# Performance work log

Hardware: AMD Instinct MI355X
Metric: run time of the kernel (lower is better)

Reference implementation:

```python
import jax, jax.numpy as jnp
import numpy as np

NB = 50000      # nb_classes (rel table is also sized by nb_classes in the source)
ES = 50         # embedding_size
D = ES + 1      # 51
B = 8192        # batch per normal-form loss
MARGIN = 0.0
REG_NORM = 1.0
INF = 5.0


def setup_inputs() -> dict:
    key = jax.random.key(0)
    ks = jax.random.split(key, 11)
    ri = lambda k, shape: jax.random.randint(k, shape, 0, NB)
    return {
        "nf1": ri(ks[0], (B, 3)),
        "nf2": ri(ks[1], (B, 3)),
        "nf3": ri(ks[2], (B, 3)),
        "nf4": ri(ks[3], (B, 3)),
        "top": ri(ks[4], (B,)),
        "nf3_neg": ri(ks[5], (B, 3)),
        "nf_inclusion": ri(ks[6], (B, 2)),
        "nf_chain": ri(ks[7], (B, 3)),
        "radius": ri(ks[8], (B,)),
        "cls_emb": jax.random.normal(ks[9], (NB, D), jnp.float32),
        "rel_emb": jax.random.normal(ks[10], (NB, D * D), jnp.float32) * 0.1,
    }


def _norm(x):
    return jnp.sqrt(jnp.sum(x * x, axis=1))


def _reg(x):
    return jnp.abs(_norm(x) - REG_NORM)


def _bmv(rm, v):  # [B,D,D] @ [B,D] -> [B,D]
    return jnp.einsum('bij,bj->bi', rm, v)


def _nf1_loss(cls_emb, rel_emb, idx):
    c = cls_emb[idx[:, 0]]
    d = cls_emb[idx[:, 2]]
    rm = rel_emb[idx[:, 1]].reshape(-1, D, D)
    cr = _bmv(rm, c)
    dr = _bmv(rm, d)
    rc = jax.nn.relu(cr[:, -1])
    rd = jax.nn.relu(dr[:, -1])
    euc = _norm(dr[:, :-1] - cr[:, :-1])
    dst = jax.nn.relu(euc + rc - rd + MARGIN)
    return dst + _reg(c[:, :-1]) + _reg(d[:, :-1])


def _nf2_loss(cls_emb, idx):
    c = cls_emb[idx[:, 0]]
    d = cls_emb[idx[:, 1]]
    e = cls_emb[idx[:, 2]]
    rc = jax.nn.relu(c[:, -1])
    rd = jax.nn.relu(d[:, -1])
    re = jax.nn.relu(e[:, -1])
    sr = rc + rd
    x1, x2, x3 = c[:, :-1], d[:, :-1], e[:, :-1]
    dst = _norm(x2 - x1)
    dst2 = _norm(x3 - x1)
    dst3 = _norm(x3 - x2)
    rdst = jax.nn.relu(jnp.minimum(rc, rd) - re - MARGIN)
    dst_loss = (jax.nn.relu(dst - sr - MARGIN)
                + jax.nn.relu(dst2 - rc - MARGIN)
                + jax.nn.relu(dst3 - rd - MARGIN)
                + rdst)
    return dst_loss + _reg(x1) + _reg(x2) + _reg(x3)


def _nf3_loss(cls_emb, rel_emb, idx):
    c = cls_emb[idx[:, 0]]
    d = cls_emb[idx[:, 2]]
    rm = rel_emb[idx[:, 1]].reshape(-1, D, D)
    cr = _bmv(rm, c)
    dr = _bmv(rm, d)
    rc = jax.nn.relu(c[:, -1])
    rd = jax.nn.relu(d[:, -1])
    euc = _norm(dr[:, :-1] - cr[:, :-1])
    dst = jax.nn.relu(euc + rc - rd - MARGIN)
    return dst + _reg(c[:, :-1]) + _reg(d[:, :-1])


def _nf4_loss(cls_emb, rel_emb, idx):
    c = cls_emb[idx[:, 1]]
    d = cls_emb[idx[:, 2]]
    rm = rel_emb[idx[:, 0]].reshape(-1, D, D)
    cr = _bmv(rm, c)
    dr = _bmv(rm, d)
    rc = jax.nn.relu(c[:, -1])
    rd = jax.nn.relu(d[:, -1])
    sr = rc + rd
    dst = _norm(dr[:, :-1] - cr[:, :-1])
    dst_loss = jax.nn.relu(dst - sr - MARGIN)
    return dst_loss + _reg(c[:, :-1]) + _reg(d[:, :-1])


def _top_loss(cls_emb, idx):
    d = cls_emb[idx]
    rd = jax.nn.relu(d[:, -1])
    return jnp.abs(rd - INF)


def _nf3_neg_loss(cls_emb, rel_emb, idx):
    c = cls_emb[idx[:, 0]]
    d = cls_emb[idx[:, 2]]
    rm = rel_emb[idx[:, 1]].reshape(-1, D, D)
    cr = _bmv(rm, c)
    dr = _bmv(rm, d)
    rc = jax.nn.relu(c[:, -1])
    rd = jax.nn.relu(d[:, -1])
    euc = _norm(dr[:, :-1] - cr[:, :-1])
    dst = -(euc - rc - rd) + MARGIN
    return dst + _reg(c[:, :-1]) + _reg(d[:, :-1])


def _chain_loss(rel_emb, idx):
    c = rel_emb[idx[:, 0]].reshape(-1, D, D)
    d = rel_emb[idx[:, 1]].reshape(-1, D, D)
    e = rel_emb[idx[:, 2]].reshape(-1, D, D)
    cd = jnp.einsum('bik,bkj->bij', c, d)
    return jnp.mean(jnp.abs(e - cd), axis=(1, 2))


def _radius_loss(cls_emb, idx):
    rd = cls_emb[idx][:, -1]
    return jnp.minimum(jnp.zeros_like(rd), rd)


def reference(nf1, nf2, nf3, nf4, top, nf3_neg, nf_inclusion, nf_chain, radius,
              cls_emb, rel_emb):
    loss1 = _nf1_loss(cls_emb, rel_emb, nf1)
    loss2 = _nf2_loss(cls_emb, nf2)
    loss3 = _nf3_loss(cls_emb, rel_emb, nf3)
    loss4 = _nf4_loss(cls_emb, rel_emb, nf4)
    loss_top = _top_loss(cls_emb, top)
    loss_neg = _nf3_neg_loss(cls_emb, rel_emb, nf3_neg)
    loss6 = _chain_loss(rel_emb, nf_chain)
    loss7 = _radius_loss(cls_emb, radius)
    loss = loss1 + loss2 + loss3 + loss4 + loss_top + loss_neg + loss6 - loss7
    return jnp.mean(loss)
```

## Files before the change

### kernel.cpp

```cpp
#include <hip/hip_runtime.h>
#include <hip/hip_bf16.h>

#define DD 51
#define DM 50
#define BB 8192
#define MM (DD*DD)
#define NBUCKET 1024

__device__ __forceinline__ float wave_sum(float v) {
    #pragma unroll
    for (int off = 32; off; off >>= 1) v += __shfl_xor(v, off);
    return v;
}

__global__ __launch_bounds__(256) void zero_kernel(float* __restrict__ buckets) {
    buckets[blockIdx.x * 256 + threadIdx.x] = 0.f;
}

__global__ __launch_bounds__(128, 8) void matvec_loss_kernel(
    const int* __restrict__ nf1, const int* __restrict__ nf3,
    const int* __restrict__ nf4, const int* __restrict__ nfneg,
    const float* __restrict__ cls,
    const float* __restrict__ rel,
    float* __restrict__ buckets)
{
    int task = blockIdx.x;
    int type = task >> 13;
    int b    = task & (BB - 1);
    int ci, ri, di;
    if (type == 0)      { ci = nf1[3*b];   ri = nf1[3*b+1];   di = nf1[3*b+2]; }
    else if (type == 1) { ci = nf3[3*b];   ri = nf3[3*b+1];   di = nf3[3*b+2]; }
    else if (type == 2) { ri = nf4[3*b];   ci = nf4[3*b+1];   di = nf4[3*b+2]; }
    else                { ci = nfneg[3*b]; ri = nfneg[3*b+1]; di = nfneg[3*b+2]; }

    __shared__ float M[MM];
    __shared__ float sc[DD], sd[DD], scr[DD], sdr[DD];
    int tid  = threadIdx.x;
    int wave = tid >> 6;
    int lane = tid & 63;

    const float* Mg = rel + (size_t)ri * MM;
    #pragma unroll 4
    for (int p = tid; p < MM; p += 128) M[p] = Mg[p];

    if (wave == 0) { if (lane < DD) sc[lane] = cls[(size_t)ci * DD + lane]; }
    else           { if (lane < DD) sd[lane] = cls[(size_t)di * DD + lane]; }
    __syncthreads();

    const float* vec = wave ? sd : sc;
    float acc = 0.f;
    if (lane < DD) {
        const float* row = &M[lane * DD];
        #pragma unroll
        for (int j = 0; j < DD; ++j) acc = fmaf(row[j], vec[j], acc);
        if (wave == 0) scr[lane] = acc; else sdr[lane] = acc;
    }
    __syncthreads();

    if (wave == 0) {
        float cv  = (lane < DM) ? sc[lane]  : 0.f;
        float dv  = (lane < DM) ? sd[lane]  : 0.f;
        float crv = (lane < DM) ? scr[lane] : 0.f;
        float drv = (lane < DM) ? sdr[lane] : 0.f;
        float t  = drv - crv;
        float e2 = wave_sum(t * t);
        float c2 = wave_sum(cv * cv);
        float d2 = wave_sum(dv * dv);
        if (lane == 0) {
            float euc = sqrtf(e2);
            float reg = fabsf(sqrtf(c2) - 1.f) + fabsf(sqrtf(d2) - 1.f);
            float L;
            if (type == 0) {
                float rc = fmaxf(scr[DM], 0.f), rd = fmaxf(sdr[DM], 0.f);
                L = fmaxf(euc + rc - rd, 0.f) + reg;
            } else if (type == 1) {
                float rc = fmaxf(sc[DM], 0.f), rd = fmaxf(sd[DM], 0.f);
                L = fmaxf(euc + rc - rd, 0.f) + reg;
            } else if (type == 2) {
                float rc = fmaxf(sc[DM], 0.f), rd = fmaxf(sd[DM], 0.f);
                L = fmaxf(euc - (rc + rd), 0.f) + reg;
            } else {
                float rc = fmaxf(sc[DM], 0.f), rd = fmaxf(sd[DM], 0.f);
                L = -(euc - rc - rd) + reg;
            }
            atomicAdd(&buckets[task & (NBUCKET - 1)], L);
        }
    }
}

__global__ __launch_bounds__(256, 4) void chain_kernel(
    const int* __restrict__ nfc,
    const float* __restrict__ rel,
    float* __restrict__ buckets)
{
    int b  = blockIdx.x;
    int ic = nfc[3*b], id = nfc[3*b+1], ie = nfc[3*b+2];
    alignas(16) __shared__ float CsT[DD][52];
    alignas(16) __shared__ float Ds [DD][52];
    const float* Cg = rel + (size_t)ic * MM;
    const float* Dg = rel + (size_t)id * MM;
    const float* Eg = rel + (size_t)ie * MM;

    int t = threadIdx.x;
    for (int p = t; p < MM; p += 256) {
        int i = p / DD, j = p - i * DD;
        CsT[j][i] = Cg[p];
        Ds [i][j] = Dg[p];
    }
    __syncthreads();

    float local = 0.f;
    if (t < 169) {
        int ti = t / 13, tj = t - ti * 13;
        int i0 = ti * 4, j0 = tj * 4;
        float acc[4][4];
        #pragma unroll
        for (int r = 0; r < 4; ++r)
            #pragma unroll
            for (int c = 0; c < 4; ++c) acc[r][c] = 0.f;

        #pragma unroll 3
        for (int k = 0; k < DD; ++k) {
            float4 ca = *(const float4*)&CsT[k][i0];
            float4 db = *(const float4*)&Ds [k][j0];
            float a[4]  = {ca.x, ca.y, ca.z, ca.w};
            float bv[4] = {db.x, db.y, db.z, db.w};
            #pragma unroll
            for (int r = 0; r < 4; ++r)
                #pragma unroll
                for (int c = 0; c < 4; ++c)
                    acc[r][c] = fmaf(a[r], bv[c], acc[r][c]);
        }
        #pragma unroll
        for (int r = 0; r < 4; ++r) {
            int i = i0 + r;
            if (i < DD) {
                #pragma unroll
                for (int c = 0; c < 4; ++c) {
                    int j = j0 + c;
                    if (j < DD)
                        local += fabsf(Eg[i * DD + j] - acc[r][c]);
                }
            }
        }
    }
    local = wave_sum(local);
    __shared__ float wsum[4];
    if ((t & 63) == 0) wsum[t >> 6] = local;
    __syncthreads();
    if (t == 0) {
        float s = (wsum[0] + wsum[1] + wsum[2] + wsum[3]) * (1.f / (float)MM);
        atomicAdd(&buckets[b & (NBUCKET - 1)], s);
    }
}

__global__ __launch_bounds__(64) void misc_kernel(
    const int* __restrict__ nf2, const int* __restrict__ top,
    const int* __restrict__ radius,
    const float* __restrict__ cls,
    float* __restrict__ buckets)
{
    int b = blockIdx.x;
    int i0 = nf2[3*b], i1 = nf2[3*b+1], i2 = nf2[3*b+2];
    int lane = threadIdx.x;
    float cv = 0.f, dv = 0.f, ev = 0.f;
    if (lane < DD) {
        cv = cls[(size_t)i0 * DD + lane];
        dv = cls[(size_t)i1 * DD + lane];
        ev = cls[(size_t)i2 * DD + lane];
    }
    float m = (lane < DM) ? 1.f : 0.f;
    float s_dc = wave_sum((dv - cv) * (dv - cv) * m);
    float s_ec = wave_sum((ev - cv) * (ev - cv) * m);
    float s_ed = wave_sum((ev - dv) * (ev - dv) * m);
    float s_c  = wave_sum(cv * cv * m);
    float s_d  = wave_sum(dv * dv * m);
    float s_e  = wave_sum(ev * ev * m);

    float c50 = __shfl(cv, DM), d50 = __shfl(dv, DM), e50 = __shfl(ev, DM);
    if (lane == 0) {
        float rc = fmaxf(c50, 0.f), rd = fmaxf(d50, 0.f), re = fmaxf(e50, 0.f);
        float L = fmaxf(sqrtf(s_dc) - (rc + rd), 0.f)
                + fmaxf(sqrtf(s_ec) - rc, 0.f)
                + fmaxf(sqrtf(s_ed) - rd, 0.f)
                + fmaxf(fminf(rc, rd) - re, 0.f)
                + fabsf(sqrtf(s_c) - 1.f)
                + fabsf(sqrtf(s_d) - 1.f)
                + fabsf(sqrtf(s_e) - 1.f);
        float t50 = cls[(size_t)top[b] * DD + DM];
        L += fabsf(fmaxf(t50, 0.f) - 5.f);
        float r50 = cls[(size_t)radius[b] * DD + DM];
        L -= fminf(r50, 0.f);
        atomicAdd(&buckets[b & (NBUCKET - 1)], L);
    }
}

__global__ __launch_bounds__(256) void finalize_kernel(
    const float* __restrict__ buckets, float* __restrict__ out)
{
    int t = threadIdx.x;
    float v = buckets[t] + buckets[t + 256] + buckets[t + 512] + buckets[t + 768];
    v = wave_sum(v);
    __shared__ float ws[4];
    if ((t & 63) == 0) ws[t >> 6] = v;
    __syncthreads();
    if (t == 0) out[0] = (ws[0] + ws[1] + ws[2] + ws[3]) * (1.f / (float)BB);
}

extern "C" void kernel_launch(void* const* d_in, const int* in_sizes, int n_in,
                              void* d_out, int out_size, void* d_ws, size_t ws_size,
                              hipStream_t stream) {
    const int* nf1     = (const int*)d_in[0];
    const int* nf2     = (const int*)d_in[1];
    const int* nf3     = (const int*)d_in[2];
    const int* nf4     = (const int*)d_in[3];
    const int* top     = (const int*)d_in[4];
    const int* nf3n    = (const int*)d_in[5];
    const int* nfc     = (const int*)d_in[7];
    const int* radius  = (const int*)d_in[8];
    const float* cls   = (const float*)d_in[9];
    const float* rel   = (const float*)d_in[10];

    float* buckets = (float*)d_ws;

    zero_kernel<<<NBUCKET / 256, 256, 0, stream>>>(buckets);
    matvec_loss_kernel<<<4 * BB, 128, 0, stream>>>(nf1, nf3, nf4, nf3n, cls, rel, buckets);
    chain_kernel<<<BB, 256, 0, stream>>>(nfc, rel, buckets);
    misc_kernel<<<BB, 64, 0, stream>>>(nf2, top, radius, cls, buckets);
    finalize_kernel<<<1, 256, 0, stream>>>(buckets, (float*)d_out);
}
```

Measured before the change: 740.1 us.

## Use linearity to do one matvec per task and shrink blocks to one wave

The matvec loss kernel now computes M·(d−c) as a single matvec, since only the difference of the two products is needed. The relation-based radius terms come from dot products with row 50. The misc normal-form work is folded into the same launch as a fifth task type. Each block is now one 64-lane wave using padded LDS rows, float4 reads and a multiply-based divide-by-51. The chain kernel also moves to one wave computing 8x8 tiles, staging the product in LDS and then reading E coalesced. The aims are fewer FMAs, fewer barriers and launches, and coalesced E reads, at the cost of more per-thread register pressure and serialised staging loads.

Result: faster. 715.6 us (-3.3%).

```diff
diff --git a/kernel.cpp b/kernel.cpp
--- a/kernel.cpp
+++ b/kernel.cpp
@@ -1,8 +1,8 @@
 #include <hip/hip_runtime.h>
-#include <hip/hip_bf16.h>
 
 #define DD 51
 #define DM 50
+#define PD 52
 #define BB 8192
 #define MM (DD*DD)
 #define NBUCKET 1024
@@ -13,186 +13,210 @@
     return v;
 }
 
+__device__ __forceinline__ int div51(int p) {
+    return (int)((((unsigned long long)(unsigned)p) * 84215046ull) >> 32);
+}
+
 __global__ __launch_bounds__(256) void zero_kernel(float* __restrict__ buckets) {
     buckets[blockIdx.x * 256 + threadIdx.x] = 0.f;
 }
 
-__global__ __launch_bounds__(128, 8) void matvec_loss_kernel(
+__global__ __launch_bounds__(64, 2) void taskA_kernel(
     const int* __restrict__ nf1, const int* __restrict__ nf3,
     const int* __restrict__ nf4, const int* __restrict__ nfneg,
+    const int* __restrict__ nf2, const int* __restrict__ top,
+    const int* __restrict__ radius,
     const float* __restrict__ cls,
     const float* __restrict__ rel,
     float* __restrict__ buckets)
 {
-    int task = blockIdx.x;
-    int type = task >> 13;
-    int b    = task & (BB - 1);
-    int ci, ri, di;
-    if (type == 0)      { ci = nf1[3*b];   ri = nf1[3*b+1];   di = nf1[3*b+2]; }
-    else if (type == 1) { ci = nf3[3*b];   ri = nf3[3*b+1];   di = nf3[3*b+2]; }
-    else if (type == 2) { ri = nf4[3*b];   ci = nf4[3*b+1];   di = nf4[3*b+2]; }
-    else                { ci = nfneg[3*b]; ri = nfneg[3*b+1]; di = nfneg[3*b+2]; }
-
-    __shared__ float M[MM];
-    __shared__ float sc[DD], sd[DD], scr[DD], sdr[DD];
-    int tid  = threadIdx.x;
-    int wave = tid >> 6;
-    int lane = tid & 63;
-
-    const float* Mg = rel + (size_t)ri * MM;
-    #pragma unroll 4
-    for (int p = tid; p < MM; p += 128) M[p] = Mg[p];
-
-    if (wave == 0) { if (lane < DD) sc[lane] = cls[(size_t)ci * DD + lane]; }
-    else           { if (lane < DD) sd[lane] = cls[(size_t)di * DD + lane]; }
-    __syncthreads();
-
-    const float* vec = wave ? sd : sc;
-    float acc = 0.f;
-    if (lane < DD) {
-        const float* row = &M[lane * DD];
+    alignas(16) __shared__ float Mw[DD * PD];
+    alignas(16) __shared__ float vb[PD];
+    const int task = blockIdx.x;
+    const int type = task >> 13;
+    const int b    = task & (BB - 1);
+    const int lane = threadIdx.x;
+
+    if (type < 4) {
+        int ci, ri, di;
+        if (type == 0)      { ci = nf1[3*b];   ri = nf1[3*b+1];   di = nf1[3*b+2]; }
+        else if (type == 1) { ci = nf3[3*b];   ri = nf3[3*b+1];   di = nf3[3*b+2]; }
+        else if (type == 2) { ri = nf4[3*b];   ci = nf4[3*b+1];   di = nf4[3*b+2]; }
+        else                { ci = nfneg[3*b]; ri = nfneg[3*b+1]; di = nfneg[3*b+2]; }
+
+        float cv = 0.f, dv = 0.f;
+        if (lane < DD) {
+            cv = cls[(size_t)ci * DD + lane];
+            dv = cls[(size_t)di * DD + lane];
+        }
+        if (lane < PD) vb[lane] = (lane < DD) ? (dv - cv) : 0.f;
+        if (lane < DD) Mw[lane * PD + (PD - 1)] = 0.f;
+
+        const float* Mg = rel + (size_t)ri * MM;
         #pragma unroll
-        for (int j = 0; j < DD; ++j) acc = fmaf(row[j], vec[j], acc);
-        if (wave == 0) scr[lane] = acc; else sdr[lane] = acc;
-    }
-    __syncthreads();
-
-    if (wave == 0) {
-        float cv  = (lane < DM) ? sc[lane]  : 0.f;
-        float dv  = (lane < DM) ? sd[lane]  : 0.f;
-        float crv = (lane < DM) ? scr[lane] : 0.f;
-        float drv = (lane < DM) ? sdr[lane] : 0.f;
-        float t  = drv - crv;
-        float e2 = wave_sum(t * t);
-        float c2 = wave_sum(cv * cv);
-        float d2 = wave_sum(dv * dv);
+        for (int k = 0; k < 40; ++k) {
+            int p = lane + (k << 6);
+            Mw[p + div51(p)] = Mg[p];
+        }
+        { int p = lane + 2560; if (p < MM) Mw[p + div51(p)] = Mg[p]; }
+        __syncthreads();
+
+        float acc = 0.f;
+        if (lane < DD) {
+            const float4* rp = (const float4*)(Mw + lane * PD);
+            const float4* vp = (const float4*)vb;
+            #pragma unroll
+            for (int q = 0; q < 13; ++q) {
+                float4 a = rp[q], w = vp[q];
+                acc = fmaf(a.x, w.x, acc);
+                acc = fmaf(a.y, w.y, acc);
+                acc = fmaf(a.z, w.z, acc);
+                acc = fmaf(a.w, w.w, acc);
+            }
+        }
+        float mk = (lane < DM) ? 1.f : 0.f;
+        float e2 = wave_sum(acc * acc * mk);
+        float c2 = wave_sum(cv * cv * mk);
+        float d2 = wave_sum(dv * dv * mk);
+        float c50 = __shfl(cv, DM);
+        float d50 = __shfl(dv, DM);
+        float s1 = 0.f, s2 = 0.f;
+        if (type == 0) {
+            float m50 = (lane < DD) ? Mw[DM * PD + lane] : 0.f;
+            s1 = wave_sum(m50 * cv);
+            s2 = wave_sum(m50 * dv);
+        }
         if (lane == 0) {
             float euc = sqrtf(e2);
             float reg = fabsf(sqrtf(c2) - 1.f) + fabsf(sqrtf(d2) - 1.f);
             float L;
             if (type == 0) {
-                float rc = fmaxf(scr[DM], 0.f), rd = fmaxf(sdr[DM], 0.f);
+                float rc = fmaxf(s1, 0.f), rd = fmaxf(s2, 0.f);
                 L = fmaxf(euc + rc - rd, 0.f) + reg;
             } else if (type == 1) {
-                float rc = fmaxf(sc[DM], 0.f), rd = fmaxf(sd[DM], 0.f);
+                float rc = fmaxf(c50, 0.f), rd = fmaxf(d50, 0.f);
                 L = fmaxf(euc + rc - rd, 0.f) + reg;
             } else if (type == 2) {
-                float rc = fmaxf(sc[DM], 0.f), rd = fmaxf(sd[DM], 0.f);
+                float rc = fmaxf(c50, 0.f), rd = fmaxf(d50, 0.f);
                 L = fmaxf(euc - (rc + rd), 0.f) + reg;
             } else {
-                float rc = fmaxf(sc[DM], 0.f), rd = fmaxf(sd[DM], 0.f);
+                float rc = fmaxf(c50, 0.f), rd = fmaxf(d50, 0.f);
                 L = -(euc - rc - rd) + reg;
             }
             atomicAdd(&buckets[task & (NBUCKET - 1)], L);
         }
-    }
-}
-
-__global__ __launch_bounds__(256, 4) void chain_kernel(
+    } else {
+        int i0 = nf2[3*b], i1 = nf2[3*b+1], i2 = nf2[3*b+2];
+        float cv = 0.f, dv = 0.f, ev = 0.f;
+        if (lane < DD) {
+            cv = cls[(size_t)i0 * DD + lane];
+            dv = cls[(size_t)i1 * DD + lane];
+            ev = cls[(size_t)i2 * DD + lane];
+        }
+        float t50 = cls[(size_t)top[b]    * DD + DM];
+        float r50 = cls[(size_t)radius[b] * DD + DM];
+        float m = (lane < DM) ? 1.f : 0.f;
+        float s_dc = wave_sum((dv - cv) * (dv - cv) * m);
+        float s_ec = wave_sum((ev - cv) * (ev - cv) * m);
+        float s_ed = wave_sum((ev - dv) * (ev - dv) * m);
+        float s_c  = wave_sum(cv * cv * m);
+        float s_d  = wave_sum(dv * dv * m);
+        float s_e  = wave_sum(ev * ev * m);
+        float c50 = __shfl(cv, DM), d50 = __shfl(dv, DM), e50 = __shfl(ev, DM);
+        if (lane == 0) {
+            float rc = fmaxf(c50, 0.f), rd = fmaxf(d50, 0.f), re = fmaxf(e50, 0.f);
+            float L = fmaxf(sqrtf(s_dc) - (rc + rd), 0.f)
+                    + fmaxf(sqrtf(s_ec) - rc, 0.f)
+                    + fmaxf(sqrtf(s_ed) - rd, 0.f)
+                    + fmaxf(fminf(rc, rd) - re, 0.f)
+                    + fabsf(sqrtf(s_c) - 1.f)
+                    + fabsf(sqrtf(s_d) - 1.f)
+                    + fabsf(sqrtf(s_e) - 1.f)
+                    + fabsf(fmaxf(t50, 0.f) - 5.f)
+                    - fminf(r50, 0.f);
+            atomicAdd(&buckets[task & (NBUCKET - 1)], L);
+        }
+    }
+}
+
+__global__ __launch_bounds__(64, 2) void chainB_kernel(
     const int* __restrict__ nfc,
     const float* __restrict__ rel,
     float* __restrict__ buckets)
 {
-    int b  = blockIdx.x;
+    alignas(16) __shared__ float lds[2 * DD * PD + 8];
+    float* CsT = lds;
+    float* Dsm = lds + DD * PD;
+    const int b    = blockIdx.x;
+    const int lane = threadIdx.x;
     int ic = nfc[3*b], id = nfc[3*b+1], ie = nfc[3*b+2];
-    alignas(16) __shared__ float CsT[DD][52];
-    alignas(16) __shared__ float Ds [DD][52];
     const float* Cg = rel + (size_t)ic * MM;
     const float* Dg = rel + (size_t)id * MM;
     const float* Eg = rel + (size_t)ie * MM;
 
-    int t = threadIdx.x;
-    for (int p = t; p < MM; p += 256) {
-        int i = p / DD, j = p - i * DD;
-        CsT[j][i] = Cg[p];
-        Ds [i][j] = Dg[p];
-    }
-    __syncthreads();
-
-    float local = 0.f;
-    if (t < 169) {
-        int ti = t / 13, tj = t - ti * 13;
-        int i0 = ti * 4, j0 = tj * 4;
-        float acc[4][4];
+    #pragma unroll 10
+    for (int t = 0; t < 40; ++t) {
+        int p = lane + (t << 6);
+        int r = div51(p), c = p - r * DD;
+        CsT[c * PD + r] = Cg[p];
+        Dsm[p + r]      = Dg[p];
+    }
+    { int p = lane + 2560;
+      if (p < MM) { int r = div51(p), c = p - r * DD; CsT[c*PD + r] = Cg[p]; Dsm[p + r] = Dg[p]; } }
+    __syncthreads();
+
+    int ti = 0, tj = 0;
+    if (lane < 49) { ti = lane / 7; tj = lane - ti * 7; }
+    const int i0 = ti * 8, j0 = tj * 8;
+    float a2[8][8];
+    #pragma unroll
+    for (int r = 0; r < 8; ++r)
         #pragma unroll
-        for (int r = 0; r < 4; ++r)
-            #pragma unroll
-            for (int c = 0; c < 4; ++c) acc[r][c] = 0.f;
-
+        for (int c = 0; c < 8; ++c) a2[r][c] = 0.f;
+
+    if (lane < 49) {
         #pragma unroll 3
         for (int k = 0; k < DD; ++k) {
-            float4 ca = *(const float4*)&CsT[k][i0];
-            float4 db = *(const float4*)&Ds [k][j0];
-            float a[4]  = {ca.x, ca.y, ca.z, ca.w};
-            float bv[4] = {db.x, db.y, db.z, db.w};
+            const float4* cp = (const float4*)(CsT + k * PD + i0);
+            const float4* dp = (const float4*)(Dsm + k * PD + j0);
+            float4 ca0 = cp[0], ca1 = cp[1];
+            float4 db0 = dp[0], db1 = dp[1];
+            float A_[8] = {ca0.x, ca0.y, ca0.z, ca0.w, ca1.x, ca1.y, ca1.z, ca1.w};
+            float B_[8] = {db0.x, db0.y, db0.z, db0.w, db1.x, db1.y, db1.z, db1.w};
             #pragma unroll
-            for (int r = 0; r < 4; ++r)
+            for (int r = 0; r < 8; ++r)
                 #pragma unroll
-                for (int c = 0; c < 4; ++c)
-                    acc[r][c] = fmaf(a[r], bv[c], acc[r][c]);
-        }
+                for (int c = 0; c < 8; ++c)
+                    a2[r][c] = fmaf(A_[r], B_[c], a2[r][c]);
+        }
+    }
+    __syncthreads();
+
+    if (lane < 49) {
         #pragma unroll
-        for (int r = 0; r < 4; ++r) {
+        for (int r = 0; r < 8; ++r) {
             int i = i0 + r;
             if (i < DD) {
-                #pragma unroll
-                for (int c = 0; c < 4; ++c) {
-                    int j = j0 + c;
-                    if (j < DD)
-                        local += fabsf(Eg[i * DD + j] - acc[r][c]);
-                }
+                *(float4*)(lds + i * PD + j0) =
+                    make_float4(a2[r][0], a2[r][1], a2[r][2], a2[r][3]);
+                if (tj < 6)
+                    *(float4*)(lds + i * PD + j0 + 4) =
+                        make_float4(a2[r][4], a2[r][5], a2[r][6], a2[r][7]);
             }
         }
     }
+    __syncthreads();
+
+    float local = 0.f;
+    #pragma unroll 10
+    for (int t = 0; t < 40; ++t) {
+        int p = lane + (t << 6);
+        local += fabsf(Eg[p] - lds[p + div51(p)]);
+    }
+    { int p = lane + 2560; if (p < MM) local += fabsf(Eg[p] - lds[p + div51(p)]); }
     local = wave_sum(local);
-    __shared__ float wsum[4];
-    if ((t & 63) == 0) wsum[t >> 6] = local;
-    __syncthreads();
-    if (t == 0) {
-        float s = (wsum[0] + wsum[1] + wsum[2] + wsum[3]) * (1.f / (float)MM);
-        atomicAdd(&buckets[b & (NBUCKET - 1)], s);
-    }
-}
-
-__global__ __launch_bounds__(64) void misc_kernel(
-    const int* __restrict__ nf2, const int* __restrict__ top,
-    const int* __restrict__ radius,
-    const float* __restrict__ cls,
-    float* __restrict__ buckets)
-{
-    int b = blockIdx.x;
-    int i0 = nf2[3*b], i1 = nf2[3*b+1], i2 = nf2[3*b+2];
-    int lane = threadIdx.x;
-    float cv = 0.f, dv = 0.f, ev = 0.f;
-    if (lane < DD) {
-        cv = cls[(size_t)i0 * DD + lane];
-        dv = cls[(size_t)i1 * DD + lane];
-        ev = cls[(size_t)i2 * DD + lane];
-    }
-    float m = (lane < DM) ? 1.f : 0.f;
-    float s_dc = wave_sum((dv - cv) * (dv - cv) * m);
-    float s_ec = wave_sum((ev - cv) * (ev - cv) * m);
-    float s_ed = wave_sum((ev - dv) * (ev - dv) * m);
-    float s_c  = wave_sum(cv * cv * m);
-    float s_d  = wave_sum(dv * dv * m);
-    float s_e  = wave_sum(ev * ev * m);
-
-    float c50 = __shfl(cv, DM), d50 = __shfl(dv, DM), e50 = __shfl(ev, DM);
-    if (lane == 0) {
-        float rc = fmaxf(c50, 0.f), rd = fmaxf(d50, 0.f), re = fmaxf(e50, 0.f);
-        float L = fmaxf(sqrtf(s_dc) - (rc + rd), 0.f)
-                + fmaxf(sqrtf(s_ec) - rc, 0.f)
-                + fmaxf(sqrtf(s_ed) - rd, 0.f)
-                + fmaxf(fminf(rc, rd) - re, 0.f)
-                + fabsf(sqrtf(s_c) - 1.f)
-                + fabsf(sqrtf(s_d) - 1.f)
-                + fabsf(sqrtf(s_e) - 1.f);
-        float t50 = cls[(size_t)top[b] * DD + DM];
-        L += fabsf(fmaxf(t50, 0.f) - 5.f);
-        float r50 = cls[(size_t)radius[b] * DD + DM];
-        L -= fminf(r50, 0.f);
-        atomicAdd(&buckets[b & (NBUCKET - 1)], L);
-    }
+    if (lane == 0)
+        atomicAdd(&buckets[b & (NBUCKET - 1)], local * (1.f / (float)MM));
 }
 
 __global__ __launch_bounds__(256) void finalize_kernel(
@@ -224,8 +248,8 @@
     float* buckets = (float*)d_ws;
 
     zero_kernel<<<NBUCKET / 256, 256, 0, stream>>>(buckets);
-    matvec_loss_kernel<<<4 * BB, 128, 0, stream>>>(nf1, nf3, nf4, nf3n, cls, rel, buckets);
-    chain_kernel<<<BB, 256, 0, stream>>>(nfc, rel, buckets);
-    misc_kernel<<<BB, 64, 0, stream>>>(nf2, top, radius, cls, buckets);
+    taskA_kernel<<<5 * BB, 64, 0, stream>>>(nf1, nf3, nf4, nf3n, nf2, top, radius,
+                                            cls, rel, buckets);
+    chainB_kernel<<<BB, 64, 0, stream>>>(nfc, rel, buckets);
     finalize_kernel<<<1, 256, 0, stream>>>(buckets, (float*)d_out);
 }
```
